# Optimization experiments

Measured on AMD Instinct MI355X. Metric: run time of the kernel, lower is better.

## Reference

```python
import jax, jax.numpy as jnp
import numpy as np

N_BINS = 15


def setup_inputs() -> dict:
    key = jax.random.key(0)
    k1, k2 = jax.random.split(key)
    N, C = 16777216, 3
    logits = jax.random.normal(k1, (N, C), dtype=jnp.float32)
    labels = jax.random.randint(k2, (N,), 0, C, dtype=jnp.int64)
    return {"logits": logits, "labels": labels}


def reference(logits, labels):
    # softmax + max over classes
    probs = jax.nn.softmax(logits, axis=1)
    confidences = jnp.max(probs, axis=1)            # [N]
    predictions = jnp.argmax(probs, axis=1)         # [N]
    accuracies = (predictions == labels).astype(logits.dtype)

    n = confidences.shape[0]
    # bin i covers (i/n_bins, (i+1)/n_bins]; first upper >= conf via side='left'
    uppers = jnp.linspace(0.0, 1.0, N_BINS + 1, dtype=logits.dtype)[1:]
    bin_idx = jnp.clip(jnp.searchsorted(uppers, confidences, side="left"), 0, N_BINS - 1)

    ones = jnp.ones_like(confidences)
    cnt = jax.ops.segment_sum(ones, bin_idx, num_segments=N_BINS)
    conf_sum = jax.ops.segment_sum(confidences, bin_idx, num_segments=N_BINS)
    acc_sum = jax.ops.segment_sum(accuracies, bin_idx, num_segments=N_BINS)

    safe_cnt = jnp.maximum(cnt, 1.0)
    gap = jnp.abs(conf_sum / safe_cnt - acc_sum / safe_cnt)
    prop = cnt / n
    ece = jnp.sum(jnp.where(cnt > 0, gap * prop, 0.0))
    return ece[None]  # shape (1,) like the torch module
```

## Files before the change

### kernel.cpp

```cpp
#include <hip/hip_runtime.h>
#include <math.h>

#define NBINS 15
#define THREADS 256
#define GRID 2048

struct Accum {
  double d[NBINS];
};

__device__ __forceinline__ void process_row(float l0, float l1, float l2, int lab,
                                            float* a) {
  float m = fmaxf(l0, fmaxf(l1, l2));
  float s = __expf(l0 - m) + __expf(l1 - m) + __expf(l2 - m);
  float conf = __fdividef(1.0f, s);
  int pred = 0;
  float best = l0;
  if (l1 > best) { pred = 1; best = l1; }
  if (l2 > best) { pred = 2; }
  float val = conf - ((pred == lab) ? 1.0f : 0.0f);
  int bin = (int)ceilf(conf * 15.0f) - 1;
  bin = bin < 4 ? 4 : (bin > NBINS - 1 ? NBINS - 1 : bin);
#pragma unroll
  for (int b = 4; b <= 14; ++b) a[b - 4] += (bin == b) ? val : 0.0f;
}

__global__ __launch_bounds__(THREADS, 6) void ece_main(
    const float4* __restrict__ logits4, const int4* __restrict__ labels4,
    Accum* __restrict__ ws, int n) {
  float a[11];
#pragma unroll
  for (int i = 0; i < 11; ++i) a[i] = 0.0f;

  const int nquads = n >> 2;
  const int total = gridDim.x * blockDim.x;
  for (int q = blockIdx.x * blockDim.x + threadIdx.x; q < nquads; q += total) {
    float4 x = logits4[3 * q + 0];
    float4 y = logits4[3 * q + 1];
    float4 z = logits4[3 * q + 2];
    int4 lb = labels4[q];
    process_row(x.x, x.y, x.z, lb.x, a);
    process_row(x.w, y.x, y.y, lb.y, a);
    process_row(y.z, y.w, z.x, lb.z, a);
    process_row(z.y, z.z, z.w, lb.w, a);
  }
  if (blockIdx.x == 0 && threadIdx.x == 0) {
    const float* lf = (const float*)logits4;
    const int* li = (const int*)labels4;
    for (int r = (n >> 2) << 2; r < n; ++r)
      process_row(lf[3 * r], lf[3 * r + 1], lf[3 * r + 2], li[r], a);
  }

#pragma unroll
  for (int i = 0; i < 11; ++i) {
    float v = a[i];
    for (int off = 32; off > 0; off >>= 1) v += __shfl_down(v, off, 64);
    a[i] = v;
  }
  __shared__ float s_part[THREADS / 64][11];
  const int wave = threadIdx.x >> 6;
  const int lane = threadIdx.x & 63;
  if (lane == 0) {
#pragma unroll
    for (int i = 0; i < 11; ++i) s_part[wave][i] = a[i];
  }
  __syncthreads();
  if (threadIdx.x < 11) {
    float v = 0.0f;
#pragma unroll
    for (int w = 0; w < THREADS / 64; ++w) v += s_part[w][threadIdx.x];
    atomicAdd(&ws->d[threadIdx.x + 4], (double)v);
  }
}

__global__ void ece_final(const Accum* __restrict__ ws, float* __restrict__ out, int n) {
  if (threadIdx.x == 0 && blockIdx.x == 0) {
    double ece = 0.0;
    for (int b = 0; b < NBINS; ++b) ece += fabs(ws->d[b]);
    out[0] = (float)(ece / (double)n);
  }
}

extern "C" void kernel_launch(void* const* d_in, const int* in_sizes, int n_in,
                              void* d_out, int out_size, void* d_ws, size_t ws_size,
                              hipStream_t stream) {
  const float4* logits4 = (const float4*)d_in[0];
  const int4* labels4 = (const int4*)d_in[1];
  const int n = in_sizes[1];
  Accum* ws = (Accum*)d_ws;
  hipMemsetAsync(d_ws, 0, sizeof(Accum), stream);
  ece_main<<<GRID, THREADS, 0, stream>>>(logits4, labels4, ws, n);
  ece_final<<<1, 64, 0, stream>>>(ws, (float*)d_out, n);
}
```

Before: 68.14 us.

## Replace register bin accumulators with per-wave shared-memory atomic histograms

Each row now adds its value to a per-wave shared-memory histogram with an atomic, instead of doing predicated adds into 11 register accumulators. Threads load two quads (8 rows) per loop iteration, and the grid is reduced. This is meant to cut ALU work and register pressure and to increase memory-level parallelism. The cost is possible heavy contention on LDS atomics, since many lanes hit the same few bins.

```diff
diff --git a/kernel.cpp b/kernel.cpp
--- a/kernel.cpp
+++ b/kernel.cpp
@@ -3,14 +3,14 @@
 
 #define NBINS 15
 #define THREADS 256
-#define GRID 2048
+#define GRID 1536
 
 struct Accum {
   double d[NBINS];
 };
 
 __device__ __forceinline__ void process_row(float l0, float l1, float l2, int lab,
-                                            float* a) {
+                                            float* h) {
   float m = fmaxf(l0, fmaxf(l1, l2));
   float s = __expf(l0 - m) + __expf(l1 - m) + __expf(l2 - m);
   float conf = __fdividef(1.0f, s);
@@ -20,56 +20,48 @@
   if (l2 > best) { pred = 2; }
   float val = conf - ((pred == lab) ? 1.0f : 0.0f);
   int bin = (int)ceilf(conf * 15.0f) - 1;
-  bin = bin < 4 ? 4 : (bin > NBINS - 1 ? NBINS - 1 : bin);
-#pragma unroll
-  for (int b = 4; b <= 14; ++b) a[b - 4] += (bin == b) ? val : 0.0f;
+  bin = bin < 0 ? 0 : (bin > NBINS - 1 ? NBINS - 1 : bin);
+  atomicAdd(&h[bin], val);
 }
 
 __global__ __launch_bounds__(THREADS, 6) void ece_main(
     const float4* __restrict__ logits4, const int4* __restrict__ labels4,
     Accum* __restrict__ ws, int n) {
-  float a[11];
-#pragma unroll
-  for (int i = 0; i < 11; ++i) a[i] = 0.0f;
+  __shared__ float hist[THREADS / 64][16];
+  if (threadIdx.x < (THREADS / 64) * 16) ((float*)hist)[threadIdx.x] = 0.0f;
+  __syncthreads();
+  float* h = hist[threadIdx.x >> 6];
 
-  const int nquads = n >> 2;
+  const int npairs = n >> 3;
   const int total = gridDim.x * blockDim.x;
-  for (int q = blockIdx.x * blockDim.x + threadIdx.x; q < nquads; q += total) {
-    float4 x = logits4[3 * q + 0];
-    float4 y = logits4[3 * q + 1];
-    float4 z = logits4[3 * q + 2];
-    int4 lb = labels4[q];
-    process_row(x.x, x.y, x.z, lb.x, a);
-    process_row(x.w, y.x, y.y, lb.y, a);
-    process_row(y.z, y.w, z.x, lb.z, a);
-    process_row(z.y, z.z, z.w, lb.w, a);
+  for (int p = blockIdx.x * blockDim.x + threadIdx.x; p < npairs; p += total) {
+    const float4* lp = logits4 + 6 * (size_t)p;
+    float4 x0 = lp[0], y0 = lp[1], z0 = lp[2];
+    float4 x1 = lp[3], y1 = lp[4], z1 = lp[5];
+    int4 la = labels4[2 * p + 0];
+    int4 lc = labels4[2 * p + 1];
+    process_row(x0.x, x0.y, x0.z, la.x, h);
+    process_row(x0.w, y0.x, y0.y, la.y, h);
+    process_row(y0.z, y0.w, z0.x, la.z, h);
+    process_row(z0.y, z0.z, z0.w, la.w, h);
+    process_row(x1.x, x1.y, x1.z, lc.x, h);
+    process_row(x1.w, y1.x, y1.y, lc.y, h);
+    process_row(y1.z, y1.w, z1.x, lc.z, h);
+    process_row(z1.y, z1.z, z1.w, lc.w, h);
   }
   if (blockIdx.x == 0 && threadIdx.x == 0) {
     const float* lf = (const float*)logits4;
     const int* li = (const int*)labels4;
-    for (int r = (n >> 2) << 2; r < n; ++r)
-      process_row(lf[3 * r], lf[3 * r + 1], lf[3 * r + 2], li[r], a);
+    for (int r = (n >> 3) << 3; r < n; ++r)
+      process_row(lf[3 * r], lf[3 * r + 1], lf[3 * r + 2], li[r], h);
   }
 
-#pragma unroll
-  for (int i = 0; i < 11; ++i) {
-    float v = a[i];
-    for (int off = 32; off > 0; off >>= 1) v += __shfl_down(v, off, 64);
-    a[i] = v;
-  }
-  __shared__ float s_part[THREADS / 64][11];
-  const int wave = threadIdx.x >> 6;
-  const int lane = threadIdx.x & 63;
-  if (lane == 0) {
-#pragma unroll
-    for (int i = 0; i < 11; ++i) s_part[wave][i] = a[i];
-  }
   __syncthreads();
-  if (threadIdx.x < 11) {
+  if (threadIdx.x < NBINS) {
     float v = 0.0f;
 #pragma unroll
-    for (int w = 0; w < THREADS / 64; ++w) v += s_part[w][threadIdx.x];
-    atomicAdd(&ws->d[threadIdx.x + 4], (double)v);
+    for (int w = 0; w < THREADS / 64; ++w) v += hist[w][threadIdx.x];
+    atomicAdd(&ws->d[threadIdx.x], (double)v);
   }
 }
 
```

Result: slower. 104.8 us (+53.8%).

## Prefetch next tile, replace atomics and memset with per-block partials

Applied to the files above, without the earlier changes.

Software-pipelines the grid-stride loop by loading the next quad of rows before processing the current one. Replaces the memset plus double-precision atomics with per-block float partials that the final kernel reduces in double, which removes the memset launch. Also uses a hardware reciprocal and a label-logit comparison instead of an explicit argmax, and raises the occupancy hint. The tie-handling for correctness differs slightly, and the extra prefetch registers may affect occupancy.

```diff
diff --git a/kernel.cpp b/kernel.cpp
--- a/kernel.cpp
+++ b/kernel.cpp
@@ -4,79 +4,103 @@
 #define NBINS 15
 #define THREADS 256
 #define GRID 2048
-
-struct Accum {
-  double d[NBINS];
-};
+#define BIN_LO 4
+#define NACC (NBINS - BIN_LO)
 
 __device__ __forceinline__ void process_row(float l0, float l1, float l2, int lab,
                                             float* a) {
   float m = fmaxf(l0, fmaxf(l1, l2));
   float s = __expf(l0 - m) + __expf(l1 - m) + __expf(l2 - m);
-  float conf = __fdividef(1.0f, s);
-  int pred = 0;
-  float best = l0;
-  if (l1 > best) { pred = 1; best = l1; }
-  if (l2 > best) { pred = 2; }
-  float val = conf - ((pred == lab) ? 1.0f : 0.0f);
+  float conf = __builtin_amdgcn_rcpf(s);
+  float lm = (lab == 1) ? l1 : ((lab == 2) ? l2 : l0);
+  float val = conf - ((lm >= m) ? 1.0f : 0.0f);
   int bin = (int)ceilf(conf * 15.0f) - 1;
-  bin = bin < 4 ? 4 : (bin > NBINS - 1 ? NBINS - 1 : bin);
+  bin = bin < BIN_LO ? BIN_LO : (bin > NBINS - 1 ? NBINS - 1 : bin);
 #pragma unroll
-  for (int b = 4; b <= 14; ++b) a[b - 4] += (bin == b) ? val : 0.0f;
+  for (int b = BIN_LO; b < NBINS; ++b) a[b - BIN_LO] += (bin == b) ? val : 0.0f;
 }
 
-__global__ __launch_bounds__(THREADS, 6) void ece_main(
+__global__ __launch_bounds__(THREADS, 8) void ece_main(
     const float4* __restrict__ logits4, const int4* __restrict__ labels4,
-    Accum* __restrict__ ws, int n) {
-  float a[11];
+    float* __restrict__ partial, int n) {
+  float a[NACC];
 #pragma unroll
-  for (int i = 0; i < 11; ++i) a[i] = 0.0f;
+  for (int i = 0; i < NACC; ++i) a[i] = 0.0f;
 
   const int nquads = n >> 2;
   const int total = gridDim.x * blockDim.x;
-  for (int q = blockIdx.x * blockDim.x + threadIdx.x; q < nquads; q += total) {
-    float4 x = logits4[3 * q + 0];
-    float4 y = logits4[3 * q + 1];
-    float4 z = logits4[3 * q + 2];
+  int q = blockIdx.x * blockDim.x + threadIdx.x;
+  if (q < nquads) {
+    float4 x = logits4[3 * (size_t)q + 0];
+    float4 y = logits4[3 * (size_t)q + 1];
+    float4 z = logits4[3 * (size_t)q + 2];
     int4 lb = labels4[q];
-    process_row(x.x, x.y, x.z, lb.x, a);
-    process_row(x.w, y.x, y.y, lb.y, a);
-    process_row(y.z, y.w, z.x, lb.z, a);
-    process_row(z.y, z.z, z.w, lb.w, a);
-  }
-  if (blockIdx.x == 0 && threadIdx.x == 0) {
-    const float* lf = (const float*)logits4;
-    const int* li = (const int*)labels4;
-    for (int r = (n >> 2) << 2; r < n; ++r)
-      process_row(lf[3 * r], lf[3 * r + 1], lf[3 * r + 2], li[r], a);
+    for (;;) {
+      const int qn = q + total;
+      const bool more = qn < nquads;
+      float4 xn, yn, zn;
+      int4 lbn;
+      if (more) {
+        xn = logits4[3 * (size_t)qn + 0];
+        yn = logits4[3 * (size_t)qn + 1];
+        zn = logits4[3 * (size_t)qn + 2];
+        lbn = labels4[qn];
+      }
+      process_row(x.x, x.y, x.z, lb.x, a);
+      process_row(x.w, y.x, y.y, lb.y, a);
+      process_row(y.z, y.w, z.x, lb.z, a);
+      process_row(z.y, z.z, z.w, lb.w, a);
+      if (!more) break;
+      x = xn; y = yn; z = zn; lb = lbn; q = qn;
+    }
   }
 
 #pragma unroll
-  for (int i = 0; i < 11; ++i) {
+  for (int i = 0; i < NACC; ++i) {
     float v = a[i];
+#pragma unroll
     for (int off = 32; off > 0; off >>= 1) v += __shfl_down(v, off, 64);
     a[i] = v;
   }
-  __shared__ float s_part[THREADS / 64][11];
+  __shared__ float s_part[THREADS / 64][NACC];
   const int wave = threadIdx.x >> 6;
   const int lane = threadIdx.x & 63;
   if (lane == 0) {
 #pragma unroll
-    for (int i = 0; i < 11; ++i) s_part[wave][i] = a[i];
+    for (int i = 0; i < NACC; ++i) s_part[wave][i] = a[i];
   }
   __syncthreads();
-  if (threadIdx.x < 11) {
+  if (threadIdx.x < NACC) {
     float v = 0.0f;
 #pragma unroll
     for (int w = 0; w < THREADS / 64; ++w) v += s_part[w][threadIdx.x];
-    atomicAdd(&ws->d[threadIdx.x + 4], (double)v);
+    partial[(size_t)threadIdx.x * gridDim.x + blockIdx.x] = v;
   }
 }
 
-__global__ void ece_final(const Accum* __restrict__ ws, float* __restrict__ out, int n) {
-  if (threadIdx.x == 0 && blockIdx.x == 0) {
+__global__ __launch_bounds__(1024) void ece_final(
+    const float* __restrict__ partial, const float* __restrict__ logits,
+    const int* __restrict__ labels, float* __restrict__ out, int n, int nblocks) {
+  __shared__ double sbin[NACC];
+  const int wave = threadIdx.x >> 6;
+  const int lane = threadIdx.x & 63;
+  if (wave < NACC) {
+    double v = 0.0;
+    for (int i = lane; i < nblocks; i += 64)
+      v += (double)partial[(size_t)wave * nblocks + i];
+#pragma unroll
+    for (int off = 32; off > 0; off >>= 1) v += __shfl_down(v, off, 64);
+    if (lane == 0) sbin[wave] = v;
+  }
+  __syncthreads();
+  if (threadIdx.x == 0) {
+    float t[NACC];
+#pragma unroll
+    for (int i = 0; i < NACC; ++i) t[i] = 0.0f;
+    for (int r = (n >> 2) << 2; r < n; ++r)
+      process_row(logits[3 * r], logits[3 * r + 1], logits[3 * r + 2], labels[r], t);
     double ece = 0.0;
-    for (int b = 0; b < NBINS; ++b) ece += fabs(ws->d[b]);
+    for (int b = 0; b < NACC; ++b) ece += fabs(sbin[b] + (double)t[b]);
     out[0] = (float)(ece / (double)n);
   }
 }
@@ -87,8 +111,8 @@
   const float4* logits4 = (const float4*)d_in[0];
   const int4* labels4 = (const int4*)d_in[1];
   const int n = in_sizes[1];
-  Accum* ws = (Accum*)d_ws;
-  hipMemsetAsync(d_ws, 0, sizeof(Accum), stream);
-  ece_main<<<GRID, THREADS, 0, stream>>>(logits4, labels4, ws, n);
-  ece_final<<<1, 64, 0, stream>>>(ws, (float*)d_out, n);
+  float* partial = (float*)d_ws;
+  ece_main<<<GRID, THREADS, 0, stream>>>(logits4, labels4, partial, n);
+  ece_final<<<1, 1024, 0, stream>>>(partial, (const float*)d_in[0],
+                                    (const int*)d_in[1], (float*)d_out, n, GRID);
 }
```

Result: faster. 58.94 us (-13.5%).
